# Kernel tuning notes

Hardware: AMD Instinct MI355X
Metric: run time of the kernel (lower is better)

Reference implementation:

```python
import jax, jax.numpy as jnp
import numpy as np

B, S, D, H = 2, 2048, 1280, 16
DEPTH = D // H  # 80


def setup_inputs() -> dict:
    key = jax.random.key(0)
    ks = jax.random.split(key, 6)
    scale = 1.0 / np.sqrt(D)
    x = jax.random.normal(ks[0], (B, S, D), dtype=jnp.float32)
    # causal mask: 1.0 where attention is disallowed (strict upper triangle)
    mask = jnp.triu(jnp.ones((S, S), dtype=jnp.float32), k=1)
    Wq = jax.random.normal(ks[1], (D, D), dtype=jnp.float32) * scale
    Wk = jax.random.normal(ks[2], (D, D), dtype=jnp.float32) * scale
    Wv = jax.random.normal(ks[3], (D, D), dtype=jnp.float32) * scale
    Wo = jax.random.normal(ks[4], (D, D), dtype=jnp.float32) * scale
    z = jnp.zeros((D,), dtype=jnp.float32)
    return {"x": x, "mask": mask, "Wq": Wq, "bq": z, "Wk": Wk, "bk": z,
            "Wv": Wv, "bv": z, "Wo": Wo, "bo": z}


def _split_heads(t):
    # [B, S, D] -> [B, H, S, depth]
    return t.reshape(B, -1, H, DEPTH).transpose(0, 2, 1, 3)


def reference(x, mask, Wq, bq, Wk, bk, Wv, bv, Wo, bo):
    q = _split_heads(x @ Wq + bq)
    k = _split_heads(x @ Wk + bk)
    v = _split_heads(x @ Wv + bv)
    # scaled dot-product attention with additive (masked * -10000) logits
    logits = jnp.einsum("bhqd,bhkd->bhqk", q, k) / jnp.sqrt(
        jnp.asarray(DEPTH, dtype=jnp.float32))
    logits = logits + mask * -10000.0  # mask broadcasts over [B, H]
    attn = jax.nn.softmax(logits, axis=-1)
    ctx = jnp.einsum("bhqk,bhkd->bhqd", attn, v)
    ctx = ctx.transpose(0, 2, 1, 3).reshape(B, -1, D)  # merge heads
    return ctx @ Wo + bo
```

## Files before the change

### kernel.cpp

```cpp
#include <hip/hip_runtime.h>

typedef unsigned short u16;
typedef __bf16 bf16;
typedef __bf16 bf16x8 __attribute__((ext_vector_type(8)));
typedef unsigned short u16x8 __attribute__((ext_vector_type(8)));
typedef unsigned short u16x4 __attribute__((ext_vector_type(4)));
typedef float f32x4 __attribute__((ext_vector_type(4)));

constexpr int B_ = 2, S_ = 2048, D_ = 1280, H_ = 16, DEPTH_ = 80;
constexpr int M_ = B_ * S_;
constexpr int QR_ = 128;

__device__ inline u16 f2b(float f) { return __builtin_bit_cast(u16, (bf16)f); }

typedef __attribute__((address_space(1))) const void gvoid;
typedef __attribute__((address_space(3))) void lvoid;
__device__ inline void gl_lds16(const void* g, void* l) {
  __builtin_amdgcn_global_load_lds((gvoid*)g, (lvoid*)l, 16, 0, 0);
}

__global__ __launch_bounds__(256) void prep_k(const float* __restrict__ x,
                                              u16* __restrict__ xbf,
                                              u16* __restrict__ QK,
                                              const float* __restrict__ W0,
                                              const float* __restrict__ W1,
                                              const float* __restrict__ W2,
                                              const float* __restrict__ W3,
                                              u16* __restrict__ WT) {
  __shared__ u16 t[32][33];
  int bid = blockIdx.x, tid = threadIdx.x;
  if (bid < 2560) {
    int i0 = (bid * 256 + tid) * 8;
    u16x8 v;
#pragma unroll
    for (int j = 0; j < 8; ++j) v[j] = f2b(x[i0 + j]);
    *(u16x8*)(xbf + i0) = v;
  } else if (bid < 5632) {
    int c = (bid - 2560) * 256 + tid;
    int r = c / 6, k = c - r * 6;
    u16x8 z = {};
    *(u16x8*)(QK + (size_t)r * QR_ + 80 + k * 8) = z;
  } else {
    int tt = bid - 5632;
    int z = tt / 1600, w = tt - z * 1600;
    int x0 = (w % 40) * 32, y0 = (w / 40) * 32;
    const float* srcs[4] = {W0, W1, W2, W3};
    const float* W = srcs[z];
    u16* out = WT + (size_t)z * D_ * D_;
    int tx = tid & 31, ty = tid >> 5;
#pragma unroll
    for (int i = 0; i < 4; ++i)
      t[ty + 8 * i][tx] = f2b(W[(size_t)(y0 + ty + 8 * i) * D_ + x0 + tx]);
    __syncthreads();
#pragma unroll
    for (int i = 0; i < 4; ++i)
      out[(size_t)(x0 + ty + 8 * i) * D_ + y0 + tx] = t[tx][ty + 8 * i];
  }
}

struct GemmAcc {
  f32x4 acc[4][4];
};
__device__ inline void gemm_core(const u16* __restrict__ A,
                                 const u16* __restrict__ BT, int m0, int n0,
                                 u16* a_s, u16* b_s, GemmAcc& g) {
  int tid = threadIdx.x, lane = tid & 63, wave = tid >> 6;
  int quad = lane >> 4, l15 = lane & 15;
  int wm = wave >> 1, wn = wave & 1;
  int r4 = lane >> 2, c4 = (lane & 3) * 8;

  for (int k0 = 0; k0 < D_; k0 += 32) {
    __syncthreads();
#pragma unroll
    for (int j = 0; j < 2; ++j) {
      int ch = wave * 2 + j;
      gl_lds16(A + (size_t)(m0 + ch * 16 + r4) * D_ + k0 + c4, a_s + ch * 512);
      gl_lds16(BT + (size_t)(n0 + ch * 16 + r4) * D_ + k0 + c4, b_s + ch * 512);
    }
    __syncthreads();
    bf16x8 af[4], bfr[4];
#pragma unroll
    for (int mt = 0; mt < 4; ++mt)
      af[mt] = *(const bf16x8*)(a_s + (wm * 64 + mt * 16 + l15) * 32 + quad * 8);
#pragma unroll
    for (int nt = 0; nt < 4; ++nt)
      bfr[nt] = *(const bf16x8*)(b_s + (wn * 64 + nt * 16 + l15) * 32 + quad * 8);
#pragma unroll
    for (int mt = 0; mt < 4; ++mt)
#pragma unroll
      for (int nt = 0; nt < 4; ++nt)
        g.acc[mt][nt] = __builtin_amdgcn_mfma_f32_16x16x32_bf16(
            af[mt], bfr[nt], g.acc[mt][nt], 0, 0, 0);
  }
}

__global__ __launch_bounds__(256, 4) void gemm_out(const u16* __restrict__ A,
                                                   const u16* __restrict__ BT,
                                                   const float* __restrict__ bias,
                                                   float* __restrict__ out) {
  __shared__ __align__(16) u16 a_s[128 * 32];
  __shared__ __align__(16) u16 b_s[128 * 32];
  int lane = threadIdx.x & 63, wave = threadIdx.x >> 6;
  int quad = lane >> 4, l15 = lane & 15;
  int wm = wave >> 1, wn = wave & 1;
  int m0 = blockIdx.y * 128, n0 = blockIdx.x * 128;

  GemmAcc g = {};
  gemm_core(A, BT, m0, n0, a_s, b_s, g);

#pragma unroll
  for (int nt = 0; nt < 4; ++nt) {
    int col = n0 + wn * 64 + nt * 16 + l15;
    float bv = bias[col];
#pragma unroll
    for (int mt = 0; mt < 4; ++mt)
#pragma unroll
      for (int r = 0; r < 4; ++r) {
        int row = m0 + wm * 64 + mt * 16 + quad * 4 + r;
        out[(size_t)row * D_ + col] = g.acc[mt][nt][r] + bv;
      }
  }
}

__device__ inline void stage_half(const u16* __restrict__ gsrc, int half,
                                  u16* lbase, int wave, int lane) {
  int rl = lane >> 3, c8 = lane & 7;
  int sc = (c8 ^ rl) << 3;
#pragma unroll
  for (int i = 0; i < 2; ++i) {
    int j = half * 16 + wave * 2 + i;
    gl_lds16(gsrc + (size_t)(j * 8 + rl) * D_ + sc, lbase + j * 512);
  }
}

__device__ inline bf16x8 frd(const u16* b, int r, int g) {
  return *(const bf16x8*)(b + r * 64 + ((g ^ (r & 7)) << 3));
}

__global__ __launch_bounds__(512, 2) void gemm_qkv8(
    const u16* __restrict__ A, const u16* __restrict__ BT,
    const float* __restrict__ bq, const float* __restrict__ bk,
    const float* __restrict__ bv, u16* __restrict__ Qw, u16* __restrict__ Kw,
    u16* __restrict__ Vw) {
  __shared__ __align__(16) u16 AS[2][256 * 64];
  __shared__ __align__(16) u16 BS[2][256 * 64];
  constexpr int BK = 64, NT = D_ / BK;
  int tid = threadIdx.x, lane = tid & 63, wave = tid >> 6;
  int quad = lane >> 4, l15 = lane & 15;
  int wm = wave >> 2, wn = wave & 3;
  int bid = blockIdx.x;
  int sw = (bid & 7) * 30 + (bid >> 3);
  int by = sw / 15, bx = sw - by * 15;
  int m0 = by * 256, n0 = bx * 256;
  const u16* Ab = A + (size_t)m0 * D_;
  const u16* Bb = BT + (size_t)n0 * D_;

  f32x4 acc[8][4] = {};

  stage_half(Ab, 0, (u16*)AS[0], wave, lane);
  stage_half(Ab, 1, (u16*)AS[0], wave, lane);
  stage_half(Bb, 0, (u16*)BS[0], wave, lane);
  stage_half(Bb, 1, (u16*)BS[0], wave, lane);
  stage_half(Bb + BK, 0, (u16*)BS[1], wave, lane);
  stage_half(Bb + BK, 1, (u16*)BS[1], wave, lane);
  asm volatile("s_waitcnt vmcnt(4)" ::: "memory");
  __builtin_amdgcn_s_barrier();

  bf16x8 a[4][2], bl[2][2], bh[2][2];
  int ra = wm * 128 + l15, rb = wn * 64 + l15;

#pragma unroll 2
  for (int T = 0; T < NT; ++T) {
    const u16* Ac = AS[T & 1];
    const u16* Bc = BS[T & 1];
    u16* An = (u16*)AS[(T + 1) & 1];
    u16* Bcur = (u16*)BS[T & 1];

#pragma unroll
    for (int mt = 0; mt < 4; ++mt)
#pragma unroll
      for (int kh = 0; kh < 2; ++kh)
        a[mt][kh] = frd(Ac, ra + mt * 16, kh * 4 + quad);
#pragma unroll
    for (int nt = 0; nt < 2; ++nt)
#pragma unroll
      for (int kh = 0; kh < 2; ++kh)
        bl[nt][kh] = frd(Bc, rb + nt * 16, kh * 4 + quad);
    if (T + 1 < NT) stage_half(Ab + (size_t)(T + 1) * BK, 0, An, wave, lane);
    asm volatile("" ::: "memory");
    __builtin_amdgcn_s_barrier();
    __builtin_amdgcn_s_setprio(1);
#pragma unroll
    for (int mt = 0; mt < 4; ++mt)
#pragma unroll
      for (int nt = 0; nt < 2; ++nt)
#pragma unroll
        for (int kh = 0; kh < 2; ++kh)
          acc[mt][nt] = __builtin_amdgcn_mfma_f32_16x16x32_bf16(
              a[mt][kh], bl[nt][kh], acc[mt][nt], 0, 0, 0);
    __builtin_amdgcn_s_setprio(0);
    asm volatile("" ::: "memory");
    __builtin_amdgcn_s_barrier();

#pragma unroll
    for (int nt = 0; nt < 2; ++nt)
#pragma unroll
      for (int kh = 0; kh < 2; ++kh)
        bh[nt][kh] = frd(Bc, rb + 32 + nt * 16, kh * 4 + quad);
    if (T + 1 < NT) stage_half(Ab + (size_t)(T + 1) * BK, 1, An, wave, lane);
    asm volatile("" ::: "memory");
    __builtin_amdgcn_s_barrier();
    __builtin_amdgcn_s_setprio(1);
#pragma unroll
    for (int mt = 0; mt < 4; ++mt)
#pragma unroll
      for (int nt = 0; nt < 2; ++nt)
#pragma unroll
        for (int kh = 0; kh < 2; ++kh)
          acc[mt][nt + 2] = __builtin_amdgcn_mfma_f32_16x16x32_bf16(
              a[mt][kh], bh[nt][kh], acc[mt][nt + 2], 0, 0, 0);
    __builtin_amdgcn_s_setprio(0);
    asm volatile("" ::: "memory");
    __builtin_amdgcn_s_barrier();

#pragma unroll
    for (int mt = 0; mt < 4; ++mt)
#pragma unroll
      for (int kh = 0; kh < 2; ++kh)
        a[mt][kh] = frd(Ac, ra + 64 + mt * 16, kh * 4 + quad);
    if (T + 2 < NT) stage_half(Bb + (size_t)(T + 2) * BK, 0, Bcur, wave, lane);
    asm volatile("" ::: "memory");
    __builtin_amdgcn_s_barrier();
    __builtin_amdgcn_s_setprio(1);
#pragma unroll
    for (int mt = 0; mt < 4; ++mt)
#pragma unroll
      for (int nt = 0; nt < 2; ++nt)
#pragma unroll
        for (int kh = 0; kh < 2; ++kh)
          acc[mt + 4][nt + 2] = __builtin_amdgcn_mfma_f32_16x16x32_bf16(
              a[mt][kh], bh[nt][kh], acc[mt + 4][nt + 2], 0, 0, 0);
    __builtin_amdgcn_s_setprio(0);
    asm volatile("" ::: "memory");
    __builtin_amdgcn_s_barrier();

    if (T + 2 < NT) stage_half(Bb + (size_t)(T + 2) * BK, 1, Bcur, wave, lane);
    asm volatile("" ::: "memory");
    __builtin_amdgcn_s_barrier();
    __builtin_amdgcn_s_setprio(1);
#pragma unroll
    for (int mt = 0; mt < 4; ++mt)
#pragma unroll
      for (int nt = 0; nt < 2; ++nt)
#pragma unroll
        for (int kh = 0; kh < 2; ++kh)
          acc[mt + 4][nt] = __builtin_amdgcn_mfma_f32_16x16x32_bf16(
              a[mt][kh], bl[nt][kh], acc[mt + 4][nt], 0, 0, 0);
    __builtin_amdgcn_s_setprio(0);
    if (T < NT - 2)
      asm volatile("s_waitcnt vmcnt(4)" ::: "memory");
    else if (T == NT - 2)
      asm volatile("s_waitcnt vmcnt(0)" ::: "memory");
    asm volatile("" ::: "memory");
    __builtin_amdgcn_s_barrier();
  }

  int mat = n0 / D_;
  if (mat == 2) {
#pragma unroll
    for (int nt = 0; nt < 4; ++nt) {
      int co = n0 + wn * 64 + nt * 16 + l15 - 2 * D_;
      float bb_ = bv[co];
      int h = co / DEPTH_, d = co % DEPTH_;
#pragma unroll
      for (int mt = 0; mt < 8; ++mt) {
        int row = m0 + wm * 128 + mt * 16 + quad * 4;
        int b = row >> 11, s = row & (S_ - 1);
        u16x4 pk;
#pragma unroll
        for (int r = 0; r < 4; ++r) pk[r] = f2b(acc[mt][nt][r] + bb_);
        *(u16x4*)(Vw + ((size_t)(b * H_ + h) * DEPTH_ + d) * S_ + s) = pk;
      }
    }
  } else {
    const float* bp = (mat == 0) ? bq : bk;
    u16* outp = mat ? Kw : Qw;
#pragma unroll
    for (int nt = 0; nt < 4; ++nt) {
      int co = n0 + wn * 64 + nt * 16 + l15 - mat * D_;
      float bb_ = bp[co];
      int h = co / DEPTH_, d = co % DEPTH_;
#pragma unroll
      for (int mt = 0; mt < 8; ++mt)
#pragma unroll
        for (int r = 0; r < 4; ++r) {
          int row = m0 + wm * 128 + mt * 16 + quad * 4 + r;
          int b = row >> 11, s = row & (S_ - 1);
          outp[((size_t)(b * H_ + h) * S_ + s) * QR_ + d] =
              f2b(acc[mt][nt][r] + bb_);
        }
    }
  }
}

__global__ __launch_bounds__(256, 4) void attn_k(const u16* __restrict__ Qp,
                                                 const u16* __restrict__ Kp,
                                                 const u16* __restrict__ VT,
                                                 u16* __restrict__ ctx) {
  constexpr float SC2 = 0.16129820f;
  __shared__ __align__(16) u16 k_lo[64 * 64];
  __shared__ __align__(16) u16 k_hi[64 * 16];
  __shared__ __align__(16) u16 vt_s[80 * 64];
  __shared__ __align__(16) u16 p_s[64 * 72];
  int tid = threadIdx.x, lane = tid & 63, wave = tid >> 6;
  int quad = lane >> 4, l15 = lane & 15;
  int bid = blockIdx.x;
  int bh = bid & 31, j = bid >> 5;
  int k_ = j >> 3, m_ = j & 7;
  int qt = (k_ == 0) ? m_ : (k_ == 1) ? 31 - m_ : (k_ == 2) ? 8 + m_ : 23 - m_;
  const u16* Qb = Qp + (size_t)bh * S_ * QR_;
  const u16* Kb = Kp + (size_t)bh * S_ * QR_;
  const u16* Vb = VT + (size_t)bh * DEPTH_ * S_;

  bf16x8 qf[3];
#pragma unroll
  for (int ks = 0; ks < 3; ++ks)
    qf[ks] = *(const bf16x8*)(Qb + (size_t)(qt * 64 + wave * 16 + l15) * QR_ +
                              ks * 32 + quad * 8);

  f32x4 acc_o[5] = {};
  float lsum[4] = {};

  for (int kt = 0; kt <= qt; ++kt) {
    int k0 = kt * 64;
    __syncthreads();
#pragma unroll
    for (int i = 0; i < 2; ++i) {
      int c = wave * 2 + i;
      int row = c * 8 + (lane >> 3);
      int sc = (lane & 7) ^ (lane >> 3);
      gl_lds16(Kb + (size_t)(k0 + row) * QR_ + sc * 8, k_lo + c * 512);
    }
    if (wave < 2) {
      int row = wave * 32 + (lane >> 1);
      gl_lds16(Kb + (size_t)(k0 + row) * QR_ + 64 + (lane & 1) * 8,
               k_hi + wave * 512);
    }
#pragma unroll
    for (int i = 0; i < 3; ++i) {
      int ch = tid + 256 * i;
      if (ch < 640) {
        int row = ch >> 3, pos = ch & 7;
        int sc = pos ^ (row & 7);
        gl_lds16(Vb + (size_t)row * S_ + k0 + sc * 8, vt_s + (ch & ~63) * 8);
      }
    }
    __syncthreads();

    f32x4 sa[4] = {};
#pragma unroll
    for (int ks = 0; ks < 2; ++ks) {
      int pa = ((ks * 4 + quad) ^ (l15 & 7)) * 8;
#pragma unroll
      for (int nt = 0; nt < 4; ++nt) {
        bf16x8 bfr = *(const bf16x8*)(k_lo + (size_t)(nt * 16 + l15) * 64 + pa);
        sa[nt] = __builtin_amdgcn_mfma_f32_16x16x32_bf16(qf[ks], bfr, sa[nt], 0, 0, 0);
      }
    }
#pragma unroll
    for (int nt = 0; nt < 4; ++nt) {
      bf16x8 bfr = {};
      if (quad < 2)
        bfr = *(const bf16x8*)(k_hi + (size_t)(nt * 16 + l15) * 16 + quad * 8);
      sa[nt] = __builtin_amdgcn_mfma_f32_16x16x32_bf16(qf[2], bfr, sa[nt], 0, 0, 0);
    }
    bool diag = (kt == qt);
#pragma unroll
    for (int nt = 0; nt < 4; ++nt)
#pragma unroll
      for (int r = 0; r < 4; ++r) {
        float p = __builtin_amdgcn_exp2f(sa[nt][r] * SC2);
        if (diag && (nt * 16 + l15) > (wave * 16 + quad * 4 + r)) p = 0.0f;
        sa[nt][r] = p;
        lsum[r] += p;
      }
    asm volatile("s_waitcnt lgkmcnt(0)" ::: "memory");
#pragma unroll
    for (int nt = 0; nt < 4; ++nt)
#pragma unroll
      for (int r = 0; r < 4; ++r)
        p_s[(wave * 16 + quad * 4 + r) * 72 + nt * 16 + l15] = f2b(sa[nt][r]);
    asm volatile("s_waitcnt lgkmcnt(0)" ::: "memory");
#pragma unroll
    for (int kk = 0; kk < 2; ++kk) {
      bf16x8 af = *(const bf16x8*)(p_s + (wave * 16 + l15) * 72 + kk * 32 + quad * 8);
#pragma unroll
      for (int d5 = 0; d5 < 5; ++d5) {
        int pv = ((kk * 4 + quad) ^ (l15 & 7)) * 8;
        bf16x8 bfr = *(const bf16x8*)(vt_s + (size_t)(d5 * 16 + l15) * 64 + pv);
        acc_o[d5] = __builtin_amdgcn_mfma_f32_16x16x32_bf16(af, bfr, acc_o[d5], 0, 0, 0);
      }
    }
  }

#pragma unroll
  for (int r = 0; r < 4; ++r)
#pragma unroll
    for (int m = 1; m < 16; m <<= 1) lsum[r] += __shfl_xor(lsum[r], m, 16);

  int b = bh >> 4, h = bh & 15;
#pragma unroll
  for (int d5 = 0; d5 < 5; ++d5)
#pragma unroll
    for (int r = 0; r < 4; ++r) {
      int s = qt * 64 + wave * 16 + quad * 4 + r;
      int col = h * DEPTH_ + d5 * 16 + l15;
      ctx[(size_t)(b * S_ + s) * D_ + col] = f2b(acc_o[d5][r] / lsum[r]);
    }
}

extern "C" void kernel_launch(void* const* d_in, const int* in_sizes, int n_in,
                              void* d_out, int out_size, void* d_ws, size_t ws_size,
                              hipStream_t stream) {
  const float* x  = (const float*)d_in[0];
  const float* Wq = (const float*)d_in[2];
  const float* bq = (const float*)d_in[3];
  const float* Wk = (const float*)d_in[4];
  const float* bk = (const float*)d_in[5];
  const float* Wv = (const float*)d_in[6];
  const float* bv = (const float*)d_in[7];
  const float* Wo = (const float*)d_in[8];
  const float* bo = (const float*)d_in[9];

  const size_t DD = (size_t)D_ * D_;
  const size_t QE = (size_t)B_ * H_ * S_ * DEPTH_;
  const size_t QP = (size_t)B_ * H_ * S_ * QR_;
  u16* xbf = (u16*)d_ws;
  u16* wT  = xbf + QE;
  u16* Qw  = wT + 4 * DD;
  u16* Kw  = Qw + QP;
  u16* Vw  = Kw + QP;
  u16* Cw  = xbf;
  size_t need = (size_t)(Vw + QE - xbf) * 2;
  if (ws_size < need) return;

  prep_k<<<12032, 256, 0, stream>>>(x, xbf, Qw, Wq, Wk, Wv, Wo, wT);
  gemm_qkv8<<<240, 512, 0, stream>>>(xbf, wT, bq, bk, bv, Qw, Kw, Vw);
  attn_k<<<1024, 256, 0, stream>>>(Qw, Kw, Vw, Cw);
  gemm_out<<<dim3(D_ / 128, M_ / 128), 256, 0, stream>>>(Cw, wT + 3 * DD, bo,
                                                         (float*)d_out);
}
```

Before: 241.5 us.

## Double-buffer K/V tiles in attention kernel to overlap loads with MFMA

Splits the K and V^T shared-memory tiles into two buffers and issues the global-to-LDS loads for the next key tile before computing on the current one. Each iteration now ends with a vmcnt wait and a barrier instead of starting with paired barriers. The goal is to hide global load latency behind the QK and PV matrix math. In exchange, LDS use roughly doubles, so launch bounds drop from 4 to 3 blocks per CU, which lowers occupancy.

```diff
diff --git a/kernel.cpp b/kernel.cpp
--- a/kernel.cpp
+++ b/kernel.cpp
@@ -303,14 +303,42 @@
   }
 }
 
-__global__ __launch_bounds__(256, 4) void attn_k(const u16* __restrict__ Qp,
+__device__ inline void attn_stage(const u16* __restrict__ Kb,
+                                  const u16* __restrict__ Vb, int k0,
+                                  u16* klo, u16* khi, u16* vs, int wave,
+                                  int lane) {
+  int tid8 = wave * 64 + lane;
+#pragma unroll
+  for (int i = 0; i < 2; ++i) {
+    int c = wave * 2 + i;
+    int row = c * 8 + (lane >> 3);
+    int sc = (lane & 7) ^ (lane >> 3);
+    gl_lds16(Kb + (size_t)(k0 + row) * QR_ + sc * 8, klo + c * 512);
+  }
+  if (wave < 2) {
+    int row = wave * 32 + (lane >> 1);
+    gl_lds16(Kb + (size_t)(k0 + row) * QR_ + 64 + (lane & 1) * 8,
+             khi + wave * 512);
+  }
+#pragma unroll
+  for (int i = 0; i < 3; ++i) {
+    int ch = tid8 + 256 * i;
+    if (ch < 640) {
+      int row = ch >> 3, pos = ch & 7;
+      int sc = pos ^ (row & 7);
+      gl_lds16(Vb + (size_t)row * S_ + k0 + sc * 8, vs + (ch & ~63) * 8);
+    }
+  }
+}
+
+__global__ __launch_bounds__(256, 3) void attn_k(const u16* __restrict__ Qp,
                                                  const u16* __restrict__ Kp,
                                                  const u16* __restrict__ VT,
                                                  u16* __restrict__ ctx) {
   constexpr float SC2 = 0.16129820f;
-  __shared__ __align__(16) u16 k_lo[64 * 64];
-  __shared__ __align__(16) u16 k_hi[64 * 16];
-  __shared__ __align__(16) u16 vt_s[80 * 64];
+  __shared__ __align__(16) u16 k_lo[2][64 * 64];
+  __shared__ __align__(16) u16 k_hi[2][64 * 16];
+  __shared__ __align__(16) u16 vt_s[2][80 * 64];
   __shared__ __align__(16) u16 p_s[64 * 72];
   int tid = threadIdx.x, lane = tid & 63, wave = tid >> 6;
   int quad = lane >> 4, l15 = lane & 15;
@@ -331,31 +359,19 @@
   f32x4 acc_o[5] = {};
   float lsum[4] = {};
 
+  attn_stage(Kb, Vb, 0, k_lo[0], k_hi[0], vt_s[0], wave, lane);
+  asm volatile("s_waitcnt vmcnt(0)" ::: "memory");
+  __syncthreads();
+
   for (int kt = 0; kt <= qt; ++kt) {
     int k0 = kt * 64;
-    __syncthreads();
-#pragma unroll
-    for (int i = 0; i < 2; ++i) {
-      int c = wave * 2 + i;
-      int row = c * 8 + (lane >> 3);
-      int sc = (lane & 7) ^ (lane >> 3);
-      gl_lds16(Kb + (size_t)(k0 + row) * QR_ + sc * 8, k_lo + c * 512);
-    }
-    if (wave < 2) {
-      int row = wave * 32 + (lane >> 1);
-      gl_lds16(Kb + (size_t)(k0 + row) * QR_ + 64 + (lane & 1) * 8,
-               k_hi + wave * 512);
-    }
-#pragma unroll
-    for (int i = 0; i < 3; ++i) {
-      int ch = tid + 256 * i;
-      if (ch < 640) {
-        int row = ch >> 3, pos = ch & 7;
-        int sc = pos ^ (row & 7);
-        gl_lds16(Vb + (size_t)row * S_ + k0 + sc * 8, vt_s + (ch & ~63) * 8);
-      }
-    }
-    __syncthreads();
+    int cur = kt & 1;
+    if (kt < qt)
+      attn_stage(Kb, Vb, k0 + 64, k_lo[cur ^ 1], k_hi[cur ^ 1], vt_s[cur ^ 1],
+                 wave, lane);
+    const u16* klo = k_lo[cur];
+    const u16* khi = k_hi[cur];
+    const u16* vsb = vt_s[cur];
 
     f32x4 sa[4] = {};
 #pragma unroll
@@ -363,7 +379,7 @@
       int pa = ((ks * 4 + quad) ^ (l15 & 7)) * 8;
 #pragma unroll
       for (int nt = 0; nt < 4; ++nt) {
-        bf16x8 bfr = *(const bf16x8*)(k_lo + (size_t)(nt * 16 + l15) * 64 + pa);
+        bf16x8 bfr = *(const bf16x8*)(klo + (size_t)(nt * 16 + l15) * 64 + pa);
         sa[nt] = __builtin_amdgcn_mfma_f32_16x16x32_bf16(qf[ks], bfr, sa[nt], 0, 0, 0);
       }
     }
@@ -371,7 +387,7 @@
     for (int nt = 0; nt < 4; ++nt) {
       bf16x8 bfr = {};
       if (quad < 2)
-        bfr = *(const bf16x8*)(k_hi + (size_t)(nt * 16 + l15) * 16 + quad * 8);
+        bfr = *(const bf16x8*)(khi + (size_t)(nt * 16 + l15) * 16 + quad * 8);
       sa[nt] = __builtin_amdgcn_mfma_f32_16x16x32_bf16(qf[2], bfr, sa[nt], 0, 0, 0);
     }
     bool diag = (kt == qt);
@@ -397,10 +413,12 @@
 #pragma unroll
       for (int d5 = 0; d5 < 5; ++d5) {
         int pv = ((kk * 4 + quad) ^ (l15 & 7)) * 8;
-        bf16x8 bfr = *(const bf16x8*)(vt_s + (size_t)(d5 * 16 + l15) * 64 + pv);
+        bf16x8 bfr = *(const bf16x8*)(vsb + (size_t)(d5 * 16 + l15) * 64 + pv);
         acc_o[d5] = __builtin_amdgcn_mfma_f32_16x16x32_bf16(af, bfr, acc_o[d5], 0, 0, 0);
       }
     }
+    asm volatile("s_waitcnt vmcnt(0)" ::: "memory");
+    __syncthreads();
   }
 
 #pragma unroll
```

New measurement: 242.1 us. Within noise of the previous version (+0.2%).
